# Performance work log

Measured on AMD Instinct MI355X. Metric: run time of the kernel, lower is better.

The kernel has to match this reference:

```python
import jax, jax.numpy as jnp
import numpy as np

N_USERS = 50000
N_PRODS = 50000
N_NODES = N_USERS + N_PRODS
N_EDGES = 600000
UD, PD, H, O = 64, 100, 128, 16


def _gcn_conv(x, W, b, src, dst, n):
    """PyG GCNConv: linear transform, add self-loops, sym-normalized scatter-add."""
    x = x @ W                                    # [n, H]
    loop = jnp.arange(n, dtype=src.dtype)
    src = jnp.concatenate([src, loop])
    dst = jnp.concatenate([dst, loop])
    deg = jax.ops.segment_sum(jnp.ones_like(dst, dtype=x.dtype), dst, num_segments=n)
    dinv = jnp.where(deg > 0, jax.lax.rsqrt(deg), 0.0)
    norm = dinv[src] * dinv[dst]                 # [E+n]
    msg = x[src] * norm[:, None]                 # gather + scale
    out = jax.ops.segment_sum(msg, dst, num_segments=n)
    return out + b


def setup_inputs() -> dict:
    key = jax.random.key(0)
    ks = jax.random.split(key, 16)
    s = 0.05
    return {
        "user_feats": jax.random.normal(ks[0], (N_USERS, UD), dtype=jnp.float32),
        "prod_feats": jax.random.normal(ks[1], (N_PRODS, PD), dtype=jnp.float32),
        "edge_index": jax.random.randint(ks[2], (2, N_EDGES), 0, N_NODES, dtype=jnp.int64),
        "Wu": jax.random.normal(ks[3], (UD, H), dtype=jnp.float32) * s,
        "bu": jnp.zeros((H,), dtype=jnp.float32),
        "Wp": jax.random.normal(ks[4], (PD, H), dtype=jnp.float32) * s,
        "bp": jnp.zeros((H,), dtype=jnp.float32),
        "W1": jax.random.normal(ks[5], (H, H), dtype=jnp.float32) * s,
        "b1": jnp.zeros((H,), dtype=jnp.float32),
        "W2": jax.random.normal(ks[6], (H, H), dtype=jnp.float32) * s,
        "b2": jnp.zeros((H,), dtype=jnp.float32),
        "W3": jax.random.normal(ks[7], (H, H), dtype=jnp.float32) * s,
        "b3": jnp.zeros((H,), dtype=jnp.float32),
        "Wo": jax.random.normal(ks[8], (H, O), dtype=jnp.float32) * s,
        "bo": jnp.zeros((O,), dtype=jnp.float32),
    }


def reference(user_feats, prod_feats, edge_index, Wu, bu, Wp, bp,
              W1, b1, W2, b2, W3, b3, Wo, bo):
    src, dst = edge_index[0], edge_index[1]
    user_x = user_feats @ Wu + bu
    prod_x = prod_feats @ Wp + bp
    x = jnp.concatenate([user_x, prod_x], axis=0)   # [N_NODES, H]
    x = jax.nn.relu(_gcn_conv(x, W1, b1, src, dst, N_NODES))
    # dropout p=0.6 is identity in eval mode
    x = jax.nn.relu(_gcn_conv(x, W2, b2, src, dst, N_NODES))
    x = jax.nn.relu(_gcn_conv(x, W3, b3, src, dst, N_NODES))
    return x @ Wo + bo                              # [N_NODES, O]
```

## Files before the change

kernel.cpp:

```cpp
#include <hip/hip_runtime.h>
#include <hip/hip_fp16.h>

#define NU 50000
#define NP 50000
#define NN 100000
#define NE 600000
#define H  128
#define O  16

typedef __attribute__((ext_vector_type(8))) _Float16 half8;
typedef __attribute__((ext_vector_type(4))) _Float16 h4v;
typedef __attribute__((ext_vector_type(4))) float f32x4;

__global__ void k_prep(const float* __restrict__ Wu, const float* __restrict__ Wp,
                       const float* __restrict__ W1, const float* __restrict__ W2,
                       const float* __restrict__ W3, const float* __restrict__ Wo,
                       const float* __restrict__ user, const float* __restrict__ prod,
                       __half* __restrict__ whU, __half* __restrict__ wlU,
                       __half* __restrict__ whP, __half* __restrict__ wlP,
                       __half* __restrict__ wh1, __half* __restrict__ wl1,
                       __half* __restrict__ wh2, __half* __restrict__ wl2,
                       __half* __restrict__ wh3, __half* __restrict__ wl3,
                       __half* __restrict__ whO, __half* __restrict__ wlO,
                       __half* __restrict__ xU, __half* __restrict__ xP,
                       int* __restrict__ cnt, int2* __restrict__ epack) {
    int idx = blockIdx.x * blockDim.x + threadIdx.x;
    if (idx >= 175784) {
        int i = idx - 175784;
        if (i < NU * 16) {
            int e = i * 4;
            float4 v = *(const float4*)(user + e);
            __half2 a = __floats2half2_rn(v.x, v.y);
            __half2 b = __floats2half2_rn(v.z, v.w);
            uint2 o; o.x = *(unsigned*)&a; o.y = *(unsigned*)&b;
            *(uint2*)(xU + e) = o;
        } else {
            int q = i - NU * 16;
            if (q >= NP * 32) return;
            int row = q >> 5, kq = (q & 31) * 4;
            float4 v;
            if (kq < 100) v = *(const float4*)(prod + row * 100 + kq);
            else { v.x = 0.f; v.y = 0.f; v.z = 0.f; v.w = 0.f; }
            __half2 a = __floats2half2_rn(v.x, v.y);
            __half2 b = __floats2half2_rn(v.z, v.w);
            uint2 o; o.x = *(unsigned*)&a; o.y = *(unsigned*)&b;
            *(uint2*)(xP + (size_t)row * 128 + kq) = o;
        }
        return;
    }
    if (idx >= 75776) {
        int i = idx - 75776;
        if (i < NN) cnt[i] = 0;
        else if (i < NN + 8) { int2 z; z.x = 0; z.y = 0; epack[NE + (i - NN)] = z; }
        return;
    }
    const float* W; __half *Wh, *Wl; int K, KPAD, NC;
    if      (idx <  8192) {              W = Wu; Wh = whU; Wl = wlU; K =  64; KPAD =  64; NC = 128; }
    else if (idx < 24576) { idx -=  8192; W = Wp; Wh = whP; Wl = wlP; K = 100; KPAD = 128; NC = 128; }
    else if (idx < 40960) { idx -= 24576; W = W1; Wh = wh1; Wl = wl1; K = 128; KPAD = 128; NC = 128; }
    else if (idx < 57344) { idx -= 40960; W = W2; Wh = wh2; Wl = wl2; K = 128; KPAD = 128; NC = 128; }
    else if (idx < 73728) { idx -= 57344; W = W3; Wh = wh3; Wl = wl3; K = 128; KPAD = 128; NC = 128; }
    else                  { idx -= 73728; W = Wo; Wh = whO; Wl = wlO; K = 128; KPAD = 128; NC =  16; }
    int n = idx / KPAD, k = idx - n * KPAD;
    float x = (k < K) ? W[k * NC + n] * 16.0f : 0.0f;
    __half h = __float2half_rn(x);
    __half l = __float2half_rn(x - __half2float(h));
    Wh[idx] = h; Wl[idx] = l;
}

__global__ void k_count(const int* __restrict__ dst, int* __restrict__ cnt,
                        int* __restrict__ rank, int E) {
    int e = blockIdx.x * blockDim.x + threadIdx.x;
    if (e < E) rank[e] = atomicAdd(&cnt[dst[e]], 1);
}

#define SCAN_TPB 256
#define SCAN_VPT 4
#define SCAN_CHUNK (SCAN_TPB * SCAN_VPT)

__global__ void k_scan1(const int* __restrict__ in, int* __restrict__ out,
                        int* __restrict__ bsums, float* __restrict__ dinv, int n) {
    __shared__ int sh[SCAN_TPB];
    int t = threadIdx.x, b = blockIdx.x;
    int base = b * SCAN_CHUNK + t * SCAN_VPT;
    int v[SCAN_VPT]; int s = 0;
#pragma unroll
    for (int i = 0; i < SCAN_VPT; i++) {
        int idx = base + i;
        v[i] = (idx < n) ? in[idx] : 0;
        if (idx < n) dinv[idx] = rsqrtf((float)(v[i] + 1));
        s += v[i];
    }
    sh[t] = s; __syncthreads();
    for (int off = 1; off < SCAN_TPB; off <<= 1) {
        int x = (t >= off) ? sh[t - off] : 0;
        __syncthreads();
        sh[t] += x;
        __syncthreads();
    }
    int run = (t > 0) ? sh[t - 1] : 0;
    if (t == SCAN_TPB - 1) bsums[b] = sh[t];
#pragma unroll
    for (int i = 0; i < SCAN_VPT; i++) {
        int idx = base + i;
        if (idx < n) out[idx] = run;
        run += v[i];
    }
}

__global__ void k_scan2(int* __restrict__ bsums, int nb) {
    __shared__ int sh[128];
    int t = threadIdx.x;
    int v = (t < nb) ? bsums[t] : 0;
    sh[t] = v; __syncthreads();
    for (int off = 1; off < 128; off <<= 1) {
        int x = (t >= off) ? sh[t - off] : 0;
        __syncthreads();
        sh[t] += x;
        __syncthreads();
    }
    if (t < nb) bsums[t] = sh[t] - v;
}

__global__ void k_fill(const int* __restrict__ src, const int* __restrict__ dst,
                       const int* __restrict__ offs, const int* __restrict__ bsums,
                       const int* __restrict__ rank, const float* __restrict__ dinv,
                       int2* __restrict__ epack, int E) {
    int e = blockIdx.x * blockDim.x + threadIdx.x;
    if (e < E) {
        int s = src[e], d = dst[e];
        int p = offs[d] + bsums[d >> 10] + rank[e];
        int2 r;
        r.x = s;
        r.y = __float_as_int(dinv[s] * dinv[d]);
        epack[p] = r;
    }
}

template <typename AT, int K, int KPAD, int NI, int MI, int NOUT, bool BIAS, bool F32OUT>
__device__ __forceinline__
void gemm_body(const AT* __restrict__ X,
               const __half* __restrict__ Wh, const __half* __restrict__ Wl,
               const float* __restrict__ bias, void* __restrict__ Cout,
               int M, int orow0, int vb) {
    constexpr int KS = KPAD / 32;
    constexpr int CSPLIT = NOUT / (16 * MI);
    const int tid  = threadIdx.x;
    const int wid  = tid >> 6, lane = tid & 63;
    const int lm   = lane & 15, q = lane >> 4;
    const int gw   = vb * 4 + wid;
    const int tile = gw / CSPLIT;
    const int c0   = (gw % CSPLIT) * (MI * 16);
    const int NT   = (M + NI * 16 - 1) / (NI * 16);
    if (tile >= NT) return;
    const int n0 = tile * (NI * 16);

    half8 wh[MI][KS], wl[MI][KS];
#pragma unroll
    for (int mi = 0; mi < MI; mi++)
#pragma unroll
        for (int ks = 0; ks < KS; ks++) {
            const size_t b = (size_t)(c0 + mi * 16 + lm) * KPAD + ks * 32 + q * 8;
            wh[mi][ks] = *(const half8*)&Wh[b];
            wl[mi][ks] = *(const half8*)&Wl[b];
        }

    f32x4 acc[NI][MI];
#pragma unroll
    for (int ni = 0; ni < NI; ni++)
#pragma unroll
        for (int mi = 0; mi < MI; mi++) acc[ni][mi] = (f32x4)0.0f;

#pragma unroll
    for (int ni = 0; ni < NI; ni++) {
        const int node = n0 + ni * 16 + lm;
        half8 xf[KS];
        if (node < M) {
#pragma unroll
            for (int ks = 0; ks < KS; ks++)
                xf[ks] = *(const half8*)((const __half*)X + (size_t)node * KPAD + ks * 32 + q * 8);
        } else {
#pragma unroll
            for (int ks = 0; ks < KS; ks++)
#pragma unroll
                for (int j = 0; j < 8; j++) xf[ks][j] = (_Float16)0.0f;
        }
#pragma unroll
        for (int ks = 0; ks < KS; ks++)
#pragma unroll
            for (int mi = 0; mi < MI; mi++) {
                acc[ni][mi] = __builtin_amdgcn_mfma_f32_16x16x32_f16(wh[mi][ks], xf[ks], acc[ni][mi], 0, 0, 0);
                acc[ni][mi] = __builtin_amdgcn_mfma_f32_16x16x32_f16(wl[mi][ks], xf[ks], acc[ni][mi], 0, 0, 0);
            }
    }

#pragma unroll
    for (int ni = 0; ni < NI; ni++) {
        const int node = n0 + ni * 16 + lm;
        if (node >= M) continue;
#pragma unroll
        for (int mi = 0; mi < MI; mi++) {
            const int cb = c0 + mi * 16 + q * 4;
            float4 bv = BIAS ? *(const float4*)&bias[cb] : make_float4(0.f, 0.f, 0.f, 0.f);
            float v0 = fmaf(acc[ni][mi][0], 0.0625f, bv.x);
            float v1 = fmaf(acc[ni][mi][1], 0.0625f, bv.y);
            float v2 = fmaf(acc[ni][mi][2], 0.0625f, bv.z);
            float v3 = fmaf(acc[ni][mi][3], 0.0625f, bv.w);
            if constexpr (F32OUT) {
                *(float4*)((float*)Cout + (size_t)(orow0 + node) * NOUT + cb) =
                    make_float4(v0, v1, v2, v3);
            } else {
                __half2 h0 = __floats2half2_rn(v0, v1);
                __half2 h1 = __floats2half2_rn(v2, v3);
                uint2 o; o.x = *(unsigned*)&h0; o.y = *(unsigned*)&h1;
                *(uint2*)((__half*)Cout + (size_t)(orow0 + node) * NOUT + cb) = o;
            }
        }
    }
}

template <typename AT, int K, int KPAD, int NI, int MI, int NOUT, bool BIAS, bool F32OUT>
__launch_bounds__(256)
__global__ void k_gemm_reg(const AT* __restrict__ X,
                           const __half* __restrict__ Wh, const __half* __restrict__ Wl,
                           const float* __restrict__ bias, void* __restrict__ Cout,
                           int M, int orow0) {
    gemm_body<AT, K, KPAD, NI, MI, NOUT, BIAS, F32OUT>(X, Wh, Wl, bias, Cout, M, orow0, blockIdx.x);
}

__launch_bounds__(256)
__global__ void k_gemm_inputs(const __half* __restrict__ xU, const __half* __restrict__ xP,
                              const __half* __restrict__ whU, const __half* __restrict__ wlU,
                              const __half* __restrict__ whP, const __half* __restrict__ wlP,
                              const float* __restrict__ bu, const float* __restrict__ bp,
                              void* __restrict__ xA, int blkU) {
    if ((int)blockIdx.x < blkU)
        gemm_body<__half,  64,  64, 2, 4, 128, true, false>(xU, whU, wlU, bu, xA, NU, 0, blockIdx.x);
    else
        gemm_body<__half, 128, 128, 2, 2, 128, true, false>(xP, whP, wlP, bp, xA, NP, NU, blockIdx.x - blkU);
}

__launch_bounds__(256)
__global__ void k_aggregate(const __half* __restrict__ y, const int* __restrict__ offs,
                            const int* __restrict__ bsums, const int2* __restrict__ epack,
                            const float* __restrict__ dinv, const float* __restrict__ bias,
                            __half* __restrict__ out) {
    const int node = __builtin_amdgcn_readfirstlane(blockIdx.x * 4 + (threadIdx.x >> 6));
    const int l = threadIdx.x & 63;
    const int h = l >> 5, j = l & 31;

    int e0 = offs[node] + bsums[node >> 10];
    int e1 = (node + 1 < NN) ? (offs[node + 1] + bsums[(node + 1) >> 10]) : NE;
    e0 = __builtin_amdgcn_readfirstlane(e0);
    e1 = __builtin_amdgcn_readfirstlane(e1);

    const h4v* y4 = (const h4v*)y;

    const float di2 = dinv[node] * dinv[node];
    h4v sv = y4[(size_t)node * 32 + j];
    float4 bv = *(const float4*)&bias[4 * j];

    f32x4 acc0 = (f32x4)0.f, acc1 = (f32x4)0.f, acc2 = (f32x4)0.f, acc3 = (f32x4)0.f;

    for (int e = e0; e < e1; e += 8) {
        const int eb = e + 4 * h;
        const int2* pe = epack + eb;
        int2 p0 = pe[0];
        int2 p1 = pe[1];
        int2 p2 = pe[2];
        int2 p3 = pe[3];
        float w0 = (eb + 0 < e1) ? __int_as_float(p0.y) : 0.f;
        float w1 = (eb + 1 < e1) ? __int_as_float(p1.y) : 0.f;
        float w2 = (eb + 2 < e1) ? __int_as_float(p2.y) : 0.f;
        float w3 = (eb + 3 < e1) ? __int_as_float(p3.y) : 0.f;
        h4v v0 = y4[(size_t)p0.x * 32 + j];
        h4v v1 = y4[(size_t)p1.x * 32 + j];
        h4v v2 = y4[(size_t)p2.x * 32 + j];
        h4v v3 = y4[(size_t)p3.x * 32 + j];
        acc0[0] = fmaf((float)v0[0], w0, acc0[0]); acc0[1] = fmaf((float)v0[1], w0, acc0[1]);
        acc0[2] = fmaf((float)v0[2], w0, acc0[2]); acc0[3] = fmaf((float)v0[3], w0, acc0[3]);
        acc1[0] = fmaf((float)v1[0], w1, acc1[0]); acc1[1] = fmaf((float)v1[1], w1, acc1[1]);
        acc1[2] = fmaf((float)v1[2], w1, acc1[2]); acc1[3] = fmaf((float)v1[3], w1, acc1[3]);
        acc2[0] = fmaf((float)v2[0], w2, acc2[0]); acc2[1] = fmaf((float)v2[1], w2, acc2[1]);
        acc2[2] = fmaf((float)v2[2], w2, acc2[2]); acc2[3] = fmaf((float)v2[3], w2, acc2[3]);
        acc3[0] = fmaf((float)v3[0], w3, acc3[0]); acc3[1] = fmaf((float)v3[1], w3, acc3[1]);
        acc3[2] = fmaf((float)v3[2], w3, acc3[2]); acc3[3] = fmaf((float)v3[3], w3, acc3[3]);
    }

    f32x4 s = (acc0 + acc1) + (acc2 + acc3);
    float t0 = s[0] + __shfl_xor(s[0], 32, 64);
    float t1 = s[1] + __shfl_xor(s[1], 32, 64);
    float t2 = s[2] + __shfl_xor(s[2], 32, 64);
    float t3 = s[3] + __shfl_xor(s[3], 32, 64);

    float r0 = fmaf((float)sv[0], di2, t0) + bv.x;
    float r1 = fmaf((float)sv[1], di2, t1) + bv.y;
    float r2 = fmaf((float)sv[2], di2, t2) + bv.z;
    float r3 = fmaf((float)sv[3], di2, t3) + bv.w;
    if (l < 32) {
        __half2 ha = __floats2half2_rn(fmaxf(r0, 0.f), fmaxf(r1, 0.f));
        __half2 hb = __floats2half2_rn(fmaxf(r2, 0.f), fmaxf(r3, 0.f));
        uint2 o; o.x = *(unsigned*)&ha; o.y = *(unsigned*)&hb;
        *(uint2*)(out + (size_t)node * H + 4 * j) = o;
    }
}

extern "C" void kernel_launch(void* const* d_in, const int* in_sizes, int n_in,
                              void* d_out, int out_size, void* d_ws, size_t ws_size,
                              hipStream_t stream) {
    const float* user = (const float*)d_in[0];
    const float* prod = (const float*)d_in[1];
    const int*   eidx = (const int*)  d_in[2];
    const int*   edst = eidx + NE;
    const int*   esrc = eidx;
    const float* Wu = (const float*)d_in[3];
    const float* bu = (const float*)d_in[4];
    const float* Wp = (const float*)d_in[5];
    const float* bp = (const float*)d_in[6];
    const float* W1 = (const float*)d_in[7];
    const float* b1 = (const float*)d_in[8];
    const float* W2 = (const float*)d_in[9];
    const float* b2 = (const float*)d_in[10];
    const float* W3 = (const float*)d_in[11];
    const float* b3 = (const float*)d_in[12];
    const float* Wo = (const float*)d_in[13];
    const float* bo = (const float*)d_in[14];
    float* out = (float*)d_out;

    char* ws = (char*)d_ws;
    size_t p = 0;
    auto alloc = [&](size_t bytes) -> void* {
        void* r = ws + p;
        p += (bytes + 255) & ~(size_t)255;
        return r;
    };
    __half* xA   = (__half*)alloc((size_t)NN * H * 2);
    __half* xB   = (__half*)alloc((size_t)NN * H * 2);
    __half* xU   = (__half*)alloc((size_t)NU * 64 * 2);
    __half* xP   = (__half*)alloc((size_t)NP * 128 * 2);
    int*   cnt   = (int*)  alloc((size_t)NN * 4);
    int*   rank  = (int*)  alloc((size_t)NE * 4);
    int*   offs  = (int*)  alloc((size_t)(NN + 1) * 4);
    float* dinv  = (float*)alloc((size_t)NN * 4);
    int2*  epack = (int2*) alloc((size_t)(NE + 8) * 8);
    int*   bsums = (int*)  alloc(128 * 4);
    __half* whU = (__half*)alloc(128 * 64 * 2);
    __half* wlU = (__half*)alloc(128 * 64 * 2);
    __half* whP = (__half*)alloc(128 * 128 * 2);
    __half* wlP = (__half*)alloc(128 * 128 * 2);
    __half* wh1 = (__half*)alloc(128 * 128 * 2);
    __half* wl1 = (__half*)alloc(128 * 128 * 2);
    __half* wh2 = (__half*)alloc(128 * 128 * 2);
    __half* wl2 = (__half*)alloc(128 * 128 * 2);
    __half* wh3 = (__half*)alloc(128 * 128 * 2);
    __half* wl3 = (__half*)alloc(128 * 128 * 2);
    __half* whO = (__half*)alloc(16 * 128 * 2);
    __half* wlO = (__half*)alloc(16 * 128 * 2);

    const int NBLK = (NN + SCAN_CHUNK - 1) / SCAN_CHUNK;

    {
        const int total = 175784 + NU * 16 + NP * 32;
        k_prep<<<(total + 255) / 256, 256, 0, stream>>>(
            Wu, Wp, W1, W2, W3, Wo, user, prod,
            whU, wlU, whP, wlP, wh1, wl1, wh2, wl2, wh3, wl3, whO, wlO,
            xU, xP, cnt, epack);
    }

    k_count<<<(NE + 255) / 256, 256, 0, stream>>>(edst, cnt, rank, NE);
    k_scan1<<<NBLK, SCAN_TPB, 0, stream>>>(cnt, offs, bsums, dinv, NN);
    k_scan2<<<1, 128, 0, stream>>>(bsums, NBLK);
    k_fill <<<(NE + 255) / 256, 256, 0, stream>>>(esrc, edst, offs, bsums, rank, dinv,
                                                  epack, NE);

    {
        constexpr int blkU = (1563 * 2 + 3) / 4;
        constexpr int blkP = (1563 * 4 + 3) / 4;
        k_gemm_inputs<<<blkU + blkP, 256, 0, stream>>>(
            xU, xP, whU, wlU, whP, wlP, bu, bp, xA, blkU);
    }

    const int blkG = (1563 * 2 + 3) / 4;
    const int blkO = (1563 + 3) / 4;

    k_gemm_reg<__half, 128, 128, 4, 4, 128, false, false><<<blkG, 256, 0, stream>>>(xA, wh1, wl1, nullptr, xB, NN, 0);
    k_aggregate<<<NN / 4, 256, 0, stream>>>(xB, offs, bsums, epack, dinv, b1, xA);
    k_gemm_reg<__half, 128, 128, 4, 4, 128, false, false><<<blkG, 256, 0, stream>>>(xA, wh2, wl2, nullptr, xB, NN, 0);
    k_aggregate<<<NN / 4, 256, 0, stream>>>(xB, offs, bsums, epack, dinv, b2, xA);
    k_gemm_reg<__half, 128, 128, 4, 4, 128, false, false><<<blkG, 256, 0, stream>>>(xA, wh3, wl3, nullptr, xB, NN, 0);
    k_aggregate<<<NN / 4, 256, 0, stream>>>(xB, offs, bsums, epack, dinv, b3, xA);

    k_gemm_reg<__half, 128, 128, 4, 1, 16, true, true><<<blkO, 256, 0, stream>>>(xA, whO, wlO, bo, out, NN, 0);
}
```

Measured before the change: 299.8 us.

## Fuse aggregation with next-layer GEMM and merge edge fill into input GEMM

Each aggregation block now handles 16 nodes, writes the relu'd fp16 rows into shared memory, and applies the next layer's weight matrix with MFMA (hi/lo split) before storing. This removes the intermediate global write and read between aggregation and the following GEMM, and drops three kernel launches. The CSR fill kernel is also merged into the input-projection GEMM launch as extra blocks. In exchange each block runs four serial aggregations per wave before the GEMM, which may lower parallelism and hide less gather latency, and the output GEMM uses only one wave per block.

```diff
diff --git a/kernel.cpp b/kernel.cpp
--- a/kernel.cpp
+++ b/kernel.cpp
@@ -122,21 +122,6 @@
     if (t < nb) bsums[t] = sh[t] - v;
 }
 
-__global__ void k_fill(const int* __restrict__ src, const int* __restrict__ dst,
-                       const int* __restrict__ offs, const int* __restrict__ bsums,
-                       const int* __restrict__ rank, const float* __restrict__ dinv,
-                       int2* __restrict__ epack, int E) {
-    int e = blockIdx.x * blockDim.x + threadIdx.x;
-    if (e < E) {
-        int s = src[e], d = dst[e];
-        int p = offs[d] + bsums[d >> 10] + rank[e];
-        int2 r;
-        r.x = s;
-        r.y = __float_as_int(dinv[s] * dinv[d]);
-        epack[p] = r;
-    }
-}
-
 template <typename AT, int K, int KPAD, int NI, int MI, int NOUT, bool BIAS, bool F32OUT>
 __device__ __forceinline__
 void gemm_body(const AT* __restrict__ X,
@@ -228,80 +213,160 @@
     gemm_body<AT, K, KPAD, NI, MI, NOUT, BIAS, F32OUT>(X, Wh, Wl, bias, Cout, M, orow0, blockIdx.x);
 }
 
+#define BLK_U 782
+#define BLK_P 1563
+#define BLK_F 2344
 __launch_bounds__(256)
-__global__ void k_gemm_inputs(const __half* __restrict__ xU, const __half* __restrict__ xP,
+__global__ void k_fill_inputs(const int* __restrict__ src, const int* __restrict__ dst,
+                              const int* __restrict__ offs, const int* __restrict__ bsums,
+                              const int* __restrict__ rank, const float* __restrict__ dinv,
+                              int2* __restrict__ epack,
+                              const __half* __restrict__ xU, const __half* __restrict__ xP,
                               const __half* __restrict__ whU, const __half* __restrict__ wlU,
                               const __half* __restrict__ whP, const __half* __restrict__ wlP,
                               const float* __restrict__ bu, const float* __restrict__ bp,
-                              void* __restrict__ xA, int blkU) {
-    if ((int)blockIdx.x < blkU)
-        gemm_body<__half,  64,  64, 2, 4, 128, true, false>(xU, whU, wlU, bu, xA, NU, 0, blockIdx.x);
-    else
-        gemm_body<__half, 128, 128, 2, 2, 128, true, false>(xP, whP, wlP, bp, xA, NP, NU, blockIdx.x - blkU);
-}
-
+                              void* __restrict__ xA) {
+    const int b = blockIdx.x;
+    if (b < BLK_U) {
+        gemm_body<__half,  64,  64, 2, 4, 128, true, false>(xU, whU, wlU, bu, xA, NU, 0, b);
+    } else if (b < BLK_U + BLK_P) {
+        gemm_body<__half, 128, 128, 2, 2, 128, true, false>(xP, whP, wlP, bp, xA, NP, NU, b - BLK_U);
+    } else {
+        int e = (b - BLK_U - BLK_P) * 256 + threadIdx.x;
+        if (e < NE) {
+            int s = src[e], d = dst[e];
+            int p = offs[d] + bsums[d >> 10] + rank[e];
+            int2 r;
+            r.x = s;
+            r.y = __float_as_int(dinv[s] * dinv[d]);
+            epack[p] = r;
+        }
+    }
+}
+
+template <int NOUT, bool F32OUT>
 __launch_bounds__(256)
-__global__ void k_aggregate(const __half* __restrict__ y, const int* __restrict__ offs,
-                            const int* __restrict__ bsums, const int2* __restrict__ epack,
-                            const float* __restrict__ dinv, const float* __restrict__ bias,
-                            __half* __restrict__ out) {
-    const int node = __builtin_amdgcn_readfirstlane(blockIdx.x * 4 + (threadIdx.x >> 6));
-    const int l = threadIdx.x & 63;
-    const int h = l >> 5, j = l & 31;
-
-    int e0 = offs[node] + bsums[node >> 10];
-    int e1 = (node + 1 < NN) ? (offs[node + 1] + bsums[(node + 1) >> 10]) : NE;
-    e0 = __builtin_amdgcn_readfirstlane(e0);
-    e1 = __builtin_amdgcn_readfirstlane(e1);
-
+__global__ void k_agg_gemm(const __half* __restrict__ y, const int* __restrict__ offs,
+                           const int* __restrict__ bsums, const int2* __restrict__ epack,
+                           const float* __restrict__ dinv, const float* __restrict__ bias_in,
+                           const __half* __restrict__ Wh, const __half* __restrict__ Wl,
+                           const float* __restrict__ bias_out, void* __restrict__ Cout) {
+    constexpr int LH = 136;
+    constexpr int MI = (NOUT == 128) ? 2 : 1;
+    __shared__ __half z[16][LH];
+    const int t   = blockIdx.x;
+    const int wid = threadIdx.x >> 6;
+    const int l   = threadIdx.x & 63;
+    const int h   = l >> 5, j = l & 31;
     const h4v* y4 = (const h4v*)y;
 
-    const float di2 = dinv[node] * dinv[node];
-    h4v sv = y4[(size_t)node * 32 + j];
-    float4 bv = *(const float4*)&bias[4 * j];
-
-    f32x4 acc0 = (f32x4)0.f, acc1 = (f32x4)0.f, acc2 = (f32x4)0.f, acc3 = (f32x4)0.f;
-
-    for (int e = e0; e < e1; e += 8) {
-        const int eb = e + 4 * h;
-        const int2* pe = epack + eb;
-        int2 p0 = pe[0];
-        int2 p1 = pe[1];
-        int2 p2 = pe[2];
-        int2 p3 = pe[3];
-        float w0 = (eb + 0 < e1) ? __int_as_float(p0.y) : 0.f;
-        float w1 = (eb + 1 < e1) ? __int_as_float(p1.y) : 0.f;
-        float w2 = (eb + 2 < e1) ? __int_as_float(p2.y) : 0.f;
-        float w3 = (eb + 3 < e1) ? __int_as_float(p3.y) : 0.f;
-        h4v v0 = y4[(size_t)p0.x * 32 + j];
-        h4v v1 = y4[(size_t)p1.x * 32 + j];
-        h4v v2 = y4[(size_t)p2.x * 32 + j];
-        h4v v3 = y4[(size_t)p3.x * 32 + j];
-        acc0[0] = fmaf((float)v0[0], w0, acc0[0]); acc0[1] = fmaf((float)v0[1], w0, acc0[1]);
-        acc0[2] = fmaf((float)v0[2], w0, acc0[2]); acc0[3] = fmaf((float)v0[3], w0, acc0[3]);
-        acc1[0] = fmaf((float)v1[0], w1, acc1[0]); acc1[1] = fmaf((float)v1[1], w1, acc1[1]);
-        acc1[2] = fmaf((float)v1[2], w1, acc1[2]); acc1[3] = fmaf((float)v1[3], w1, acc1[3]);
-        acc2[0] = fmaf((float)v2[0], w2, acc2[0]); acc2[1] = fmaf((float)v2[1], w2, acc2[1]);
-        acc2[2] = fmaf((float)v2[2], w2, acc2[2]); acc2[3] = fmaf((float)v2[3], w2, acc2[3]);
-        acc3[0] = fmaf((float)v3[0], w3, acc3[0]); acc3[1] = fmaf((float)v3[1], w3, acc3[1]);
-        acc3[2] = fmaf((float)v3[2], w3, acc3[2]); acc3[3] = fmaf((float)v3[3], w3, acc3[3]);
-    }
-
-    f32x4 s = (acc0 + acc1) + (acc2 + acc3);
-    float t0 = s[0] + __shfl_xor(s[0], 32, 64);
-    float t1 = s[1] + __shfl_xor(s[1], 32, 64);
-    float t2 = s[2] + __shfl_xor(s[2], 32, 64);
-    float t3 = s[3] + __shfl_xor(s[3], 32, 64);
-
-    float r0 = fmaf((float)sv[0], di2, t0) + bv.x;
-    float r1 = fmaf((float)sv[1], di2, t1) + bv.y;
-    float r2 = fmaf((float)sv[2], di2, t2) + bv.z;
-    float r3 = fmaf((float)sv[3], di2, t3) + bv.w;
-    if (l < 32) {
-        __half2 ha = __floats2half2_rn(fmaxf(r0, 0.f), fmaxf(r1, 0.f));
-        __half2 hb = __floats2half2_rn(fmaxf(r2, 0.f), fmaxf(r3, 0.f));
-        uint2 o; o.x = *(unsigned*)&ha; o.y = *(unsigned*)&hb;
-        *(uint2*)(out + (size_t)node * H + 4 * j) = o;
+#pragma unroll
+    for (int n = 0; n < 4; n++) {
+        const int row  = wid * 4 + n;
+        const int node = __builtin_amdgcn_readfirstlane(t * 16 + row);
+        int e0 = offs[node] + bsums[node >> 10];
+        int e1 = (node + 1 < NN) ? (offs[node + 1] + bsums[(node + 1) >> 10]) : NE;
+        e0 = __builtin_amdgcn_readfirstlane(e0);
+        e1 = __builtin_amdgcn_readfirstlane(e1);
+
+        const float di2 = dinv[node] * dinv[node];
+        h4v sv = y4[(size_t)node * 32 + j];
+        float4 bv = *(const float4*)&bias_in[4 * j];
+
+        f32x4 acc0 = (f32x4)0.f, acc1 = (f32x4)0.f, acc2 = (f32x4)0.f, acc3 = (f32x4)0.f;
+        for (int e = e0; e < e1; e += 8) {
+            const int eb = e + 4 * h;
+            const int2* pe = epack + eb;
+            int2 p0 = pe[0];
+            int2 p1 = pe[1];
+            int2 p2 = pe[2];
+            int2 p3 = pe[3];
+            float w0 = (eb + 0 < e1) ? __int_as_float(p0.y) : 0.f;
+            float w1 = (eb + 1 < e1) ? __int_as_float(p1.y) : 0.f;
+            float w2 = (eb + 2 < e1) ? __int_as_float(p2.y) : 0.f;
+            float w3 = (eb + 3 < e1) ? __int_as_float(p3.y) : 0.f;
+            h4v v0 = y4[(size_t)p0.x * 32 + j];
+            h4v v1 = y4[(size_t)p1.x * 32 + j];
+            h4v v2 = y4[(size_t)p2.x * 32 + j];
+            h4v v3 = y4[(size_t)p3.x * 32 + j];
+            acc0[0] = fmaf((float)v0[0], w0, acc0[0]); acc0[1] = fmaf((float)v0[1], w0, acc0[1]);
+            acc0[2] = fmaf((float)v0[2], w0, acc0[2]); acc0[3] = fmaf((float)v0[3], w0, acc0[3]);
+            acc1[0] = fmaf((float)v1[0], w1, acc1[0]); acc1[1] = fmaf((float)v1[1], w1, acc1[1]);
+            acc1[2] = fmaf((float)v1[2], w1, acc1[2]); acc1[3] = fmaf((float)v1[3], w1, acc1[3]);
+            acc2[0] = fmaf((float)v2[0], w2, acc2[0]); acc2[1] = fmaf((float)v2[1], w2, acc2[1]);
+            acc2[2] = fmaf((float)v2[2], w2, acc2[2]); acc2[3] = fmaf((float)v2[3], w2, acc2[3]);
+            acc3[0] = fmaf((float)v3[0], w3, acc3[0]); acc3[1] = fmaf((float)v3[1], w3, acc3[1]);
+            acc3[2] = fmaf((float)v3[2], w3, acc3[2]); acc3[3] = fmaf((float)v3[3], w3, acc3[3]);
+        }
+
+        f32x4 s = (acc0 + acc1) + (acc2 + acc3);
+        float t0 = s[0] + __shfl_xor(s[0], 32, 64);
+        float t1 = s[1] + __shfl_xor(s[1], 32, 64);
+        float t2 = s[2] + __shfl_xor(s[2], 32, 64);
+        float t3 = s[3] + __shfl_xor(s[3], 32, 64);
+
+        float r0 = fmaf((float)sv[0], di2, t0) + bv.x;
+        float r1 = fmaf((float)sv[1], di2, t1) + bv.y;
+        float r2 = fmaf((float)sv[2], di2, t2) + bv.z;
+        float r3 = fmaf((float)sv[3], di2, t3) + bv.w;
+        if (l < 32) {
+            __half2 ha = __floats2half2_rn(fmaxf(r0, 0.f), fmaxf(r1, 0.f));
+            __half2 hb = __floats2half2_rn(fmaxf(r2, 0.f), fmaxf(r3, 0.f));
+            uint2 o; o.x = *(unsigned*)&ha; o.y = *(unsigned*)&hb;
+            *(uint2*)&z[row][4 * j] = o;
+        }
+    }
+
+    const int lm = l & 15, q = l >> 4;
+    const int c0 = (NOUT == 128) ? wid * 32 : 0;
+    half8 wh[MI][4], wl[MI][4];
+    const bool active = (NOUT == 128) || (wid == 0);
+    if (active) {
+#pragma unroll
+        for (int mi = 0; mi < MI; mi++)
+#pragma unroll
+            for (int ks = 0; ks < 4; ks++) {
+                const size_t b = (size_t)(c0 + mi * 16 + lm) * 128 + ks * 32 + q * 8;
+                wh[mi][ks] = *(const half8*)&Wh[b];
+                wl[mi][ks] = *(const half8*)&Wl[b];
+            }
+    }
+    __syncthreads();
+    if (!active) return;
+
+    half8 xf[4];
+#pragma unroll
+    for (int ks = 0; ks < 4; ks++)
+        xf[ks] = *(const half8*)&z[lm][ks * 32 + q * 8];
+
+    f32x4 acc[MI];
+#pragma unroll
+    for (int mi = 0; mi < MI; mi++) acc[mi] = (f32x4)0.0f;
+#pragma unroll
+    for (int ks = 0; ks < 4; ks++)
+#pragma unroll
+        for (int mi = 0; mi < MI; mi++) {
+            acc[mi] = __builtin_amdgcn_mfma_f32_16x16x32_f16(wh[mi][ks], xf[ks], acc[mi], 0, 0, 0);
+            acc[mi] = __builtin_amdgcn_mfma_f32_16x16x32_f16(wl[mi][ks], xf[ks], acc[mi], 0, 0, 0);
+        }
+
+    const int node = t * 16 + lm;
+#pragma unroll
+    for (int mi = 0; mi < MI; mi++) {
+        const int cb = c0 + mi * 16 + q * 4;
+        float4 bv = F32OUT ? *(const float4*)&bias_out[cb] : make_float4(0.f, 0.f, 0.f, 0.f);
+        float v0 = fmaf(acc[mi][0], 0.0625f, bv.x);
+        float v1 = fmaf(acc[mi][1], 0.0625f, bv.y);
+        float v2 = fmaf(acc[mi][2], 0.0625f, bv.z);
+        float v3 = fmaf(acc[mi][3], 0.0625f, bv.w);
+        if constexpr (F32OUT) {
+            *(float4*)((float*)Cout + (size_t)node * NOUT + cb) = make_float4(v0, v1, v2, v3);
+        } else {
+            __half2 h0 = __floats2half2_rn(v0, v1);
+            __half2 h1 = __floats2half2_rn(v2, v3);
+            uint2 o; o.x = *(unsigned*)&h0; o.y = *(unsigned*)&h1;
+            *(uint2*)((__half*)Cout + (size_t)node * NOUT + cb) = o;
+        }
     }
 }
 
@@ -370,25 +435,16 @@
     k_count<<<(NE + 255) / 256, 256, 0, stream>>>(edst, cnt, rank, NE);
     k_scan1<<<NBLK, SCAN_TPB, 0, stream>>>(cnt, offs, bsums, dinv, NN);
     k_scan2<<<1, 128, 0, stream>>>(bsums, NBLK);
-    k_fill <<<(NE + 255) / 256, 256, 0, stream>>>(esrc, edst, offs, bsums, rank, dinv,
-                                                  epack, NE);
-
-    {
-        constexpr int blkU = (1563 * 2 + 3) / 4;
-        constexpr int blkP = (1563 * 4 + 3) / 4;
-        k_gemm_inputs<<<blkU + blkP, 256, 0, stream>>>(
-            xU, xP, whU, wlU, whP, wlP, bu, bp, xA, blkU);
-    }
+
+    k_fill_inputs<<<BLK_U + BLK_P + BLK_F, 256, 0, stream>>>(
+        esrc, edst, offs, bsums, rank, dinv, epack,
+        xU, xP, whU, wlU, whP, wlP, bu, bp, xA);
 
     const int blkG = (1563 * 2 + 3) / 4;
-    const int blkO = (1563 + 3) / 4;
-
     k_gemm_reg<__half, 128, 128, 4, 4, 128, false, false><<<blkG, 256, 0, stream>>>(xA, wh1, wl1, nullptr, xB, NN, 0);
-    k_aggregate<<<NN / 4, 256, 0, stream>>>(xB, offs, bsums, epack, dinv, b1, xA);
-    k_gemm_reg<__half, 128, 128, 4, 4, 128, false, false><<<blkG, 256, 0, stream>>>(xA, wh2, wl2, nullptr, xB, NN, 0);
-    k_aggregate<<<NN / 4, 256, 0, stream>>>(xB, offs, bsums, epack, dinv, b2, xA);
-    k_gemm_reg<__half, 128, 128, 4, 4, 128, false, false><<<blkG, 256, 0, stream>>>(xA, wh3, wl3, nullptr, xB, NN, 0);
-    k_aggregate<<<NN / 4, 256, 0, stream>>>(xB, offs, bsums, epack, dinv, b3, xA);
-
-    k_gemm_reg<__half, 128, 128, 4, 1, 16, true, true><<<blkO, 256, 0, stream>>>(xA, whO, wlO, bo, out, NN, 0);
-}
+
+    const int blkF = NN / 16;
+    k_agg_gemm<128, false><<<blkF, 256, 0, stream>>>(xB, offs, bsums, epack, dinv, b1, wh2, wl2, nullptr, xA);
+    k_agg_gemm<128, false><<<blkF, 256, 0, stream>>>(xA, offs, bsums, epack, dinv, b2, wh3, wl3, nullptr, xB);
+    k_agg_gemm<16,  true ><<<blkF, 256, 0, stream>>>(xB, offs, bsums, epack, dinv, b3, whO, wlO, bo, out);
+}
```

Result: slower. 306.6 us (+2.3%).
